# Kernel tuning notes

Hardware: AMD Instinct MI355X
Metric: run time of the kernel (lower is better)

Reference implementation:

```python
import jax, jax.numpy as jnp
import numpy as np

FEAT_STRIDE = 8  # features are at 1/8 image resolution -> disparity step 8 px


def feature_vol(ref, tgt, D):
    """HSMNet.feature_vol (leftview=True), fully vectorized.

    ref, tgt: [B, C, H, W] left/right feature maps.
    Returns cost: [B, C, D, H, W] where
      cost[:, :, i, :, w] = |ref[:, :, :, w] - tgt[:, :, :, w - i]| for w >= i, else 0.
    """
    B, C, H, W = ref.shape
    d = jnp.arange(D)
    w = jnp.arange(W)
    idx = w[None, :] - d[:, None]            # [D, W] source column in target
    valid = (idx >= 0)                       # [D, W]
    tgt_g = jnp.take(tgt, jnp.clip(idx, 0), axis=3)          # [B, C, H, D, W]
    diff = jnp.abs(ref[:, :, :, None, :] - tgt_g)            # [B, C, H, D, W]
    cost = jnp.where(valid[None, None, None, :, :], diff, jnp.zeros((), diff.dtype))
    return jnp.transpose(cost, (0, 1, 3, 2, 4))              # [B, C, D, H, W]


def disparity_regression(prob, stride):
    """disparityregression: expectation over disparity candidates.

    prob: [B, D, H, W] softmax over disparity axis.
    """
    D = prob.shape[1]
    disp = (jnp.arange(D) * stride).astype(prob.dtype)       # [D]
    return jnp.einsum('bdhw,d->bhw', prob, disp)             # [B, H, W]


def setup_inputs() -> dict:
    key = jax.random.key(0)
    k1, k2 = jax.random.split(key)
    B, C, H, W = 2, 32, 96, 160
    left_fea = jax.random.normal(k1, (B, C, H, W), dtype=jnp.float32)
    right_fea = jax.random.normal(k2, (B, C, H, W), dtype=jnp.float32)
    return {"left_fea": left_fea, "right_fea": right_fea, "maxdisp": 384}


def reference(left_fea, right_fea, maxdisp):
    D = maxdisp // 8  # disparity bins at 1/8 resolution (feat3 level)
    cost = feature_vol(left_fea, right_fea, D)               # [B, C, D, H, W]
    # Channel aggregation to a matching score per disparity (stands in for the
    # 3D-conv decoder, which is not defined in the provided source). Negative
    # abs-diff so that better matches get larger score before softmax.
    score = -jnp.sum(cost, axis=1)                           # [B, D, H, W]
    prob = jax.nn.softmax(score, axis=1)
    pred = disparity_regression(prob, FEAT_STRIDE)           # [B, H, W]
    return pred
```

## Files before the change

kernel.cpp:

```cpp
#include <hip/hip_runtime.h>


#define BB   2
#define CC   32
#define HH   96
#define WW   160
#define DD   48
#define TILE 32
#define NT   5
#define PARTS 8
#define DPP  6
#define TGTC 80
#define STR  33

__global__ __launch_bounds__(256, 4)
void hsm_disp_kernel(const float* __restrict__ ref,
                     const float* __restrict__ tgt,
                     float* __restrict__ out)
{
    __shared__ float tgt_l[TGTC * STR];
    __shared__ float ref_l[TILE * STR];
    __shared__ float pm [PARTS * TILE];
    __shared__ float ps [PARTS * TILE];
    __shared__ float pws[PARTS * TILE];

    int bx = blockIdx.x;
    int wg = (bx & 7) * 120 + (bx >> 3);

    int t  = wg % NT;
    int bh = wg / NT;
    int w0 = t * TILE;

    const size_t cstride = (size_t)HH * WW;
    const size_t base    = (size_t)(bh / HH) * CC * cstride + (size_t)(bh % HH) * WW;

    for (int i = threadIdx.x; i < TGTC * CC; i += 256) {
        int c  = i / TGTC;
        int ct = i - c * TGTC;
        int gc = w0 - 48 + ct;
        float v = 0.0f;
        if (gc >= 0) v = tgt[base + (size_t)c * cstride + gc];
        tgt_l[ct * STR + c] = v;
    }
    for (int i = threadIdx.x; i < TILE * CC; i += 256) {
        int c  = i >> 5;
        int cl = i & 31;
        ref_l[cl * STR + c] = ref[base + (size_t)c * cstride + (w0 + cl)];
    }
    __syncthreads();

    const int cl = threadIdx.x & 31;
    const int p  = threadIdx.x >> 5;

    float r[CC];
    #pragma unroll
    for (int c = 0; c < CC; ++c) r[c] = ref_l[cl * STR + c];

    float sc[DPP];
    #pragma unroll
    for (int j = 0; j < DPP; ++j) {
        int d  = p * DPP + j;
        int ct = cl - d + 48;
        const float* tl = &tgt_l[ct * STR];
        float acc = 0.0f;
        #pragma unroll
        for (int c = 0; c < CC; ++c)
            acc += fabsf(r[c] - tl[c]);
        sc[j] = ((w0 + cl) >= d) ? -acc : 0.0f;
    }

    float m = sc[0];
    #pragma unroll
    for (int j = 1; j < DPP; ++j) m = fmaxf(m, sc[j]);
    float s = 0.0f, ws = 0.0f;
    #pragma unroll
    for (int j = 0; j < DPP; ++j) {
        float e = __expf(sc[j] - m);
        s  += e;
        ws += e * (float)((p * DPP + j) * 8);
    }
    pm [p * TILE + cl] = m;
    ps [p * TILE + cl] = s;
    pws[p * TILE + cl] = ws;
    __syncthreads();

    if (threadIdx.x < TILE) {
        float M = pm[cl];
        #pragma unroll
        for (int q = 1; q < PARTS; ++q) M = fmaxf(M, pm[q * TILE + cl]);
        float S = 0.0f, WS = 0.0f;
        #pragma unroll
        for (int q = 0; q < PARTS; ++q) {
            float f = __expf(pm[q * TILE + cl] - M);
            S  += ps [q * TILE + cl] * f;
            WS += pws[q * TILE + cl] * f;
        }
        out[(size_t)bh * WW + w0 + cl] = WS / S;
    }
}

extern "C" void kernel_launch(void* const* d_in, const int* in_sizes, int n_in,
                              void* d_out, int out_size, void* d_ws, size_t ws_size,
                              hipStream_t stream) {
    const float* left  = (const float*)d_in[0];
    const float* right = (const float*)d_in[1];
    float* out = (float*)d_out;
    (void)in_sizes; (void)n_in; (void)out_size; (void)d_ws; (void)ws_size;

    hsm_disp_kernel<<<dim3(BB * HH * NT), dim3(256), 0, stream>>>(left, right, out);
}
```

Before: 68.84 us.

## Use 512 threads with 3 disparities each, float4 LDS reads, batched global loads

```diff
diff --git a/kernel.cpp b/kernel.cpp
--- a/kernel.cpp
+++ b/kernel.cpp
@@ -1,101 +1,116 @@
 #include <hip/hip_runtime.h>
 
 
-#define BB   2
-#define CC   32
+#define CCH  32
 #define HH   96
 #define WW   160
 #define DD   48
 #define TILE 32
 #define NT   5
-#define PARTS 8
-#define DPP  6
-#define TGTC 80
-#define STR  33
+#define PARTS 16
+#define DPP  3
+#define WIN  80
+#define STR  36
+#define NBLK (2 * HH * NT)
 
-__global__ __launch_bounds__(256, 4)
-void hsm_disp_kernel(const float* __restrict__ ref,
-                     const float* __restrict__ tgt,
+__global__ __launch_bounds__(512, 4)
+void hsm_disp_kernel(const float* __restrict__ refp,
+                     const float* __restrict__ tgtp,
                      float* __restrict__ out)
 {
-    __shared__ float tgt_l[TGTC * STR];
+    __shared__ float tgt_l[WIN * STR];
     __shared__ float ref_l[TILE * STR];
     __shared__ float pm [PARTS * TILE];
     __shared__ float ps [PARTS * TILE];
     __shared__ float pws[PARTS * TILE];
 
     int bx = blockIdx.x;
-    int wg = (bx & 7) * 120 + (bx >> 3);
+    int wg = (bx & 7) * (NBLK / 8) + (bx >> 3);
 
     int t  = wg % NT;
     int bh = wg / NT;
     int w0 = t * TILE;
 
-    const size_t cstride = (size_t)HH * WW;
-    const size_t base    = (size_t)(bh / HH) * CC * cstride + (size_t)(bh % HH) * WW;
+    const size_t cs   = (size_t)HH * WW;
+    const size_t base = (size_t)(bh / HH) * CCH * cs + (size_t)(bh % HH) * WW;
 
-    for (int i = threadIdx.x; i < TGTC * CC; i += 256) {
-        int c  = i / TGTC;
-        int ct = i - c * TGTC;
+    const int tid = threadIdx.x;
+
+    float tv[5]; int tct[5], tcc[5];
+    #pragma unroll
+    for (int k = 0; k < 5; ++k) {
+        int i  = tid + k * 512;
+        int c  = i / WIN;
+        int ct = i - c * WIN;
         int gc = w0 - 48 + ct;
-        float v = 0.0f;
-        if (gc >= 0) v = tgt[base + (size_t)c * cstride + gc];
-        tgt_l[ct * STR + c] = v;
+        tct[k] = ct; tcc[k] = c;
+        tv[k] = (gc >= 0) ? tgtp[base + (size_t)c * cs + gc] : 0.0f;
     }
-    for (int i = threadIdx.x; i < TILE * CC; i += 256) {
+    float rv2[2]; int rct[2], rcc[2];
+    #pragma unroll
+    for (int k = 0; k < 2; ++k) {
+        int i  = tid + k * 512;
         int c  = i >> 5;
-        int cl = i & 31;
-        ref_l[cl * STR + c] = ref[base + (size_t)c * cstride + (w0 + cl)];
+        int ct = i & 31;
+        rct[k] = ct; rcc[k] = c;
+        rv2[k] = refp[base + (size_t)c * cs + (w0 + ct)];
     }
+    #pragma unroll
+    for (int k = 0; k < 5; ++k) tgt_l[tct[k] * STR + tcc[k]] = tv[k];
+    #pragma unroll
+    for (int k = 0; k < 2; ++k) ref_l[rct[k] * STR + rcc[k]] = rv2[k];
     __syncthreads();
 
-    const int cl = threadIdx.x & 31;
-    const int p  = threadIdx.x >> 5;
+    const int cl = tid & 31;
+    const int p  = tid >> 5;
+    const int d0 = p * DPP;
+    const int w  = w0 + cl;
 
-    float r[CC];
+    const int ct0 = cl - d0 + 48;
+    const float4* tq0 = (const float4*)&tgt_l[(ct0    ) * STR];
+    const float4* tq1 = (const float4*)&tgt_l[(ct0 - 1) * STR];
+    const float4* tq2 = (const float4*)&tgt_l[(ct0 - 2) * STR];
+    const float4* rb  = (const float4*)&ref_l[cl * STR];
+
+    float a0 = 0.f, a1 = 0.f, a2 = 0.f;
     #pragma unroll
-    for (int c = 0; c < CC; ++c) r[c] = ref_l[cl * STR + c];
+    for (int cq = 0; cq < CCH / 4; ++cq) {
+        float4 rv = rb[cq];
+        float4 t0 = tq0[cq];
+        float4 t1 = tq1[cq];
+        float4 t2 = tq2[cq];
+        a0 += fabsf(rv.x - t0.x) + fabsf(rv.y - t0.y)
+            + fabsf(rv.z - t0.z) + fabsf(rv.w - t0.w);
+        a1 += fabsf(rv.x - t1.x) + fabsf(rv.y - t1.y)
+            + fabsf(rv.z - t1.z) + fabsf(rv.w - t1.w);
+        a2 += fabsf(rv.x - t2.x) + fabsf(rv.y - t2.y)
+            + fabsf(rv.z - t2.z) + fabsf(rv.w - t2.w);
+    }
+    float s0 = (w >= d0)     ? -a0 : 0.f;
+    float s1 = (w >= d0 + 1) ? -a1 : 0.f;
+    float s2 = (w >= d0 + 2) ? -a2 : 0.f;
 
-    float sc[DPP];
-    #pragma unroll
-    for (int j = 0; j < DPP; ++j) {
-        int d  = p * DPP + j;
-        int ct = cl - d + 48;
-        const float* tl = &tgt_l[ct * STR];
-        float acc = 0.0f;
-        #pragma unroll
-        for (int c = 0; c < CC; ++c)
-            acc += fabsf(r[c] - tl[c]);
-        sc[j] = ((w0 + cl) >= d) ? -acc : 0.0f;
-    }
-
-    float m = sc[0];
-    #pragma unroll
-    for (int j = 1; j < DPP; ++j) m = fmaxf(m, sc[j]);
-    float s = 0.0f, ws = 0.0f;
-    #pragma unroll
-    for (int j = 0; j < DPP; ++j) {
-        float e = __expf(sc[j] - m);
-        s  += e;
-        ws += e * (float)((p * DPP + j) * 8);
-    }
+    float m  = fmaxf(fmaxf(s0, s1), s2);
+    float e0 = __expf(s0 - m), e1 = __expf(s1 - m), e2 = __expf(s2 - m);
     pm [p * TILE + cl] = m;
-    ps [p * TILE + cl] = s;
-    pws[p * TILE + cl] = ws;
+    ps [p * TILE + cl] = e0 + e1 + e2;
+    pws[p * TILE + cl] = e0 * (float)(8 * d0)
+                       + e1 * (float)(8 * (d0 + 1))
+                       + e2 * (float)(8 * (d0 + 2));
     __syncthreads();
 
-    if (threadIdx.x < TILE) {
-        float M = pm[cl];
+    if (tid < TILE) {
+        float M = pm[tid];
         #pragma unroll
-        for (int q = 1; q < PARTS; ++q) M = fmaxf(M, pm[q * TILE + cl]);
-        float S = 0.0f, WS = 0.0f;
+        for (int q = 1; q < PARTS; ++q) M = fmaxf(M, pm[q * TILE + tid]);
+        float S = 0.f, WS = 0.f;
         #pragma unroll
         for (int q = 0; q < PARTS; ++q) {
-            float f = __expf(pm[q * TILE + cl] - M);
-            S  += ps [q * TILE + cl] * f;
-            WS += pws[q * TILE + cl] * f;
+            float f = __expf(pm[q * TILE + tid] - M);
+            S  += ps [q * TILE + tid] * f;
+            WS += pws[q * TILE + tid] * f;
         }
-        out[(size_t)bh * WW + w0 + cl] = WS / S;
+        out[(size_t)bh * WW + w0 + tid] = WS / S;
     }
 }
 
@@ -104,8 +119,8 @@
                               hipStream_t stream) {
     const float* left  = (const float*)d_in[0];
     const float* right = (const float*)d_in[1];
-    float* out = (float*)d_out;
+    float* outp = (float*)d_out;
     (void)in_sizes; (void)n_in; (void)out_size; (void)d_ws; (void)ws_size;
 
-    hsm_disp_kernel<<<dim3(BB * HH * NT), dim3(256), 0, stream>>>(left, right, out);
+    hsm_disp_kernel<<<dim3(NBLK), dim3(512), 0, stream>>>(left, right, outp);
 }
```

Measured after the change: 62.94 us. 1.09x faster.
